# Performance work log

Measured on AMD Instinct MI355X. Metric: run time of the kernel, lower is better.

Reference implementation:

```python
import jax, jax.numpy as jnp
import numpy as np


def gcn_conv(x, edge_index, W, b):
    """PyG GCNConv: add self-loops, symmetric deg^{-1/2} normalization,
    linear transform, then scatter-add aggregation, plus bias."""
    n = x.shape[0]
    loops = jnp.arange(n, dtype=edge_index.dtype)
    src = jnp.concatenate([edge_index[0], loops])  # [E+N]
    dst = jnp.concatenate([edge_index[1], loops])
    ones = jnp.ones(src.shape[0], dtype=x.dtype)
    deg = jax.ops.segment_sum(ones, dst, num_segments=n)  # in-degree incl. self-loop
    dinv = jax.lax.rsqrt(jnp.maximum(deg, 1e-12))
    norm = dinv[src] * dinv[dst]  # [E+N]
    h = x @ W  # transform first (out_dim <= in_dim), [N, out]
    msg = h[src] * norm[:, None]  # gather + scale
    out = jax.ops.segment_sum(msg, dst, num_segments=n)  # scatter-add
    return out + b


def setup_inputs() -> dict:
    key = jax.random.key(0)
    ks = jax.random.split(key, 8)
    N, E, D_IN, D_OUT = 100000, 6400000, 32, 4
    x = jax.random.normal(ks[0], (N, D_IN), dtype=jnp.float32)
    edge_index = jax.random.randint(ks[1], (2, E), 0, N, dtype=jnp.int64)
    s1 = 1.0 / np.sqrt(D_IN)
    s2 = 1.0 / np.sqrt(16)
    s3 = 1.0 / np.sqrt(8)
    W1 = jax.random.uniform(ks[2], (D_IN, 16), jnp.float32, -s1, s1)
    b1 = jnp.zeros((16,), jnp.float32)
    W2 = jax.random.uniform(ks[3], (16, 8), jnp.float32, -s2, s2)
    b2 = jnp.zeros((8,), jnp.float32)
    Wfc = jax.random.uniform(ks[4], (8, D_OUT), jnp.float32, -s3, s3)
    bfc = jax.random.uniform(ks[5], (D_OUT,), jnp.float32, -s3, s3)
    return {"x": x, "edge_index": edge_index, "W1": W1, "b1": b1,
            "W2": W2, "b2": b2, "Wfc": Wfc, "bfc": bfc}


def reference(x, edge_index, W1, b1, W2, b2, Wfc, bfc):
    h = jax.nn.relu(gcn_conv(x, edge_index, W1, b1))
    h = jax.nn.relu(gcn_conv(h, edge_index, W2, b2))
    return h @ Wfc + bfc
```

## Files before the change

### kernel.cpp

```cpp
#include <hip/hip_runtime.h>
#include <hip/hip_fp16.h>

#define BLK 256
#define SHIFT 8
#define BSZ 256
#define MAXB 512
#define SRCBITS 17
#define SRCMASK ((1u << SRCBITS) - 1u)
#define TILE2 8192
#define BT 512
#define LCAP 18432


__global__ __launch_bounds__(BT) void k_binA2(const int* __restrict__ src,
                                              const int* __restrict__ dst, int E, int N,
                                              unsigned* __restrict__ binned,
                                              int* __restrict__ bofs) {
    __shared__ int cnt[MAXB];
    __shared__ int sscan[MAXB];
    __shared__ int excl[MAXB];
    __shared__ unsigned sw[TILE2];
    int t = threadIdx.x;
    cnt[t] = 0;
    __syncthreads();
    size_t tb = (size_t)blockIdx.x * TILE2;
    unsigned wv[16];
    int rkbk[16];
#pragma unroll
    for (int q = 0; q < 4; ++q) {
        int i4 = t + q * BT;
        size_t e0 = tb + (size_t)i4 * 4;
        int4 s4, d4;
        bool vec = (e0 + 4 <= (size_t)E);
        if (vec) {
            s4 = ((const int4*)src)[tb / 4 + i4];
            d4 = ((const int4*)dst)[tb / 4 + i4];
        }
#pragma unroll
        for (int j = 0; j < 4; ++j) {
            int idx = q * 4 + j;
            rkbk[idx] = -1;
            size_t e = e0 + j;
            int d = -1, s = -1;
            if (vec) {
                d = (j == 0) ? d4.x : (j == 1) ? d4.y : (j == 2) ? d4.z : d4.w;
                s = (j == 0) ? s4.x : (j == 1) ? s4.y : (j == 2) ? s4.z : s4.w;
            } else if (e < (size_t)E) {
                d = dst[e]; s = src[e];
            }
            if ((unsigned)d < (unsigned)N && (unsigned)s < (unsigned)N) {
                int b = d >> SHIFT;
                wv[idx] = (unsigned)s | ((unsigned)(d & (BSZ - 1)) << SRCBITS);
                int r = atomicAdd(&cnt[b], 1);
                rkbk[idx] = (r << 9) | b;
            }
        }
    }
    __syncthreads();
    sscan[t] = cnt[t];
    __syncthreads();
    for (int off = 1; off < MAXB; off <<= 1) {
        int u = (t >= off) ? sscan[t - off] : 0;
        __syncthreads();
        sscan[t] += u;
        __syncthreads();
    }
    excl[t] = sscan[t] - cnt[t];
    __syncthreads();
    int total = sscan[MAXB - 1];
#pragma unroll
    for (int idx = 0; idx < 16; ++idx) {
        int rb = rkbk[idx];
        if (rb >= 0) sw[excl[rb & 511] + (rb >> 9)] = wv[idx];
    }
    __syncthreads();
    for (int p = t; p < total; p += BT) binned[tb + p] = sw[p];
    size_t bo = (size_t)blockIdx.x * (MAXB + 1);
    bofs[bo + t] = excl[t];
    if (t == 0) bofs[bo + MAXB] = total;
}

__global__ __launch_bounds__(MAXB) void k_bsum(const int* __restrict__ bofs, int ntiles,
                                               int* __restrict__ btot) {
    int t = threadIdx.x;
    int c = 0;
    for (int tl = blockIdx.x; tl < ntiles; tl += gridDim.x) {
        size_t bo = (size_t)tl * (MAXB + 1);
        c += bofs[bo + t + 1] - bofs[bo + t];
    }
    if (c) atomicAdd(&btot[t], c);
}

__global__ __launch_bounds__(MAXB) void k_bscan(const int* __restrict__ btot,
                                                int* __restrict__ base) {
    __shared__ int s[MAXB];
    int t = threadIdx.x;
    int v = btot[t];
    s[t] = v;
    __syncthreads();
    for (int off = 1; off < MAXB; off <<= 1) {
        int u = (t >= off) ? s[t - off] : 0;
        __syncthreads();
        s[t] += u;
        __syncthreads();
    }
    base[t] = s[t] - v;
    if (t == MAXB - 1) base[MAXB] = s[t];
}


__global__ __launch_bounds__(1024) void k_buildB4(const unsigned* __restrict__ binned,
                                                  const int* __restrict__ bofs,
                                                  const int* __restrict__ baseB,
                                                  int ntiles, int N,
                                                  float* __restrict__ dinv,
                                                  int* __restrict__ rp,
                                                  unsigned* __restrict__ csr) {
    __shared__ int h[BSZ];
    __shared__ int sc[BSZ];
    __shared__ int cnt[BSZ];
    extern __shared__ unsigned lcsr[];
    int b = blockIdx.x;
    int t = threadIdx.x;
    int gb = b << SHIFT;
    if (t < BSZ) h[t] = 0;
    __syncthreads();
    int lane = t & 63, wid = t >> 6;
    int sub = lane >> 4, sl = lane & 15;
    for (int S = wid * 4 + sub; S < ntiles; S += 64) {
        size_t bo = (size_t)S * (MAXB + 1);
        int st = bofs[bo + b], en = bofs[bo + b + 1];
        size_t base = (size_t)S * TILE2;
        for (int k = st + sl; k < en; k += 16)
            atomicAdd(&h[binned[base + k] >> SRCBITS], 1);
    }
    __syncthreads();
    if (t < BSZ) sc[t] = h[t];
    __syncthreads();
    for (int off = 1; off < BSZ; off <<= 1) {
        int u = 0;
        if (t < BSZ && t >= off) u = sc[t - off];
        __syncthreads();
        if (t < BSZ) sc[t] += u;
        __syncthreads();
    }
    int bb = baseB[b];
    int total = sc[BSZ - 1];
    if (t < BSZ) {
        int v = h[t];
        int excl = sc[t] - v;
        int gnode = gb + t;
        if (gnode < N) {
            rp[gnode] = bb + excl;
            dinv[gnode] = rsqrtf((float)v + 1.0f);
        }
        if (t == BSZ - 1) {
            int endn = gb + BSZ;
            if (endn > N) endn = N;
            rp[endn] = bb + total;
        }
        cnt[t] = excl;
    }
    __syncthreads();
    bool big = (total > LCAP);
    for (int S = wid * 4 + sub; S < ntiles; S += 64) {
        size_t bo = (size_t)S * (MAXB + 1);
        int st = bofs[bo + b], en = bofs[bo + b + 1];
        size_t base = (size_t)S * TILE2;
        for (int k = st + sl; k < en; k += 16) {
            unsigned v = binned[base + k];
            int node = v >> SRCBITS;
            int pos = atomicAdd(&cnt[node], 1);
            if (!big) lcsr[pos] = v & SRCMASK;
            else      csr[bb + pos] = v & SRCMASK;
        }
    }
    __syncthreads();
    if (!big) {
        for (int p = t; p < total; p += 1024) csr[bb + p] = lcsr[p];
    }
}


union Pk8 { __half h[8]; uint4 u; };
union H2U { unsigned u; __half2 h; };

__global__ __launch_bounds__(BLK) void k_transform1h(const float* __restrict__ x,
                                                     const float* __restrict__ W1,
                                                     const float* __restrict__ dinv,
                                                     __half* __restrict__ g1h, int N) {
    __shared__ float sW[32 * 16];
    for (int t = threadIdx.x; t < 512; t += BLK) sW[t] = W1[t];
    __syncthreads();
    int i = blockIdx.x * BLK + threadIdx.x;
    if (i >= N) return;
    float xr[32];
    const float4* xp = (const float4*)(x + (size_t)i * 32);
#pragma unroll
    for (int q = 0; q < 8; ++q) {
        float4 v = xp[q];
        xr[4*q] = v.x; xr[4*q+1] = v.y; xr[4*q+2] = v.z; xr[4*q+3] = v.w;
    }
    float di = dinv[i];
    Pk8 p0, p1;
#pragma unroll
    for (int j = 0; j < 16; ++j) {
        float a = 0.f;
#pragma unroll
        for (int k = 0; k < 32; ++k) a += xr[k] * sW[k * 16 + j];
        if (j < 8) p0.h[j] = __float2half_rn(a * di);
        else       p1.h[j - 8] = __float2half_rn(a * di);
    }
    uint4* gp = (uint4*)(g1h + (size_t)i * 16);
    gp[0] = p0.u;
    gp[1] = p1.u;
}


__global__ __launch_bounds__(BLK) void k_agg1(const int* __restrict__ rp,
                                              const unsigned* __restrict__ csr,
                                              const __half* __restrict__ g1h,
                                              const float* __restrict__ dinv,
                                              const float* __restrict__ b1,
                                              const float* __restrict__ W2,
                                              float* __restrict__ g2, int N) {
    __shared__ float sW[16 * 8];
    __shared__ float sb[16];
    if (threadIdx.x < 128) sW[threadIdx.x] = W2[threadIdx.x];
    if (threadIdx.x < 16) sb[threadIdx.x] = b1[threadIdx.x];
    __syncthreads();
    int wid = blockIdx.x * (BLK / 64) + (threadIdx.x >> 6);
    if (wid >= N) return;
    int lane = threadIdx.x & 63;
    int c4 = lane & 3;
    int slot = lane >> 2;
    int base_ = rp[wid], end = rp[wid + 1];
    float a0 = 0.f, a1 = 0.f, a2 = 0.f, a3 = 0.f;
    int k = base_ + slot;
    for (; k + 16 < end; k += 32) {
        unsigned s0 = csr[k], s1 = csr[k + 16];
        uint2 u0 = *(const uint2*)(g1h + (size_t)s0 * 16 + (c4 << 2));
        uint2 u1 = *(const uint2*)(g1h + (size_t)s1 * 16 + (c4 << 2));
        H2U x0, x1, y0, y1;
        x0.u = u0.x; y0.u = u0.y; x1.u = u1.x; y1.u = u1.y;
        float2 f0 = __half22float2(x0.h), f1 = __half22float2(y0.h);
        float2 f2 = __half22float2(x1.h), f3 = __half22float2(y1.h);
        a0 += f0.x + f2.x; a1 += f0.y + f2.y;
        a2 += f1.x + f3.x; a3 += f1.y + f3.y;
    }
    if (k < end) {
        unsigned s0 = csr[k];
        uint2 u0 = *(const uint2*)(g1h + (size_t)s0 * 16 + (c4 << 2));
        H2U x0, y0;
        x0.u = u0.x; y0.u = u0.y;
        float2 f0 = __half22float2(x0.h), f1 = __half22float2(y0.h);
        a0 += f0.x; a1 += f0.y; a2 += f1.x; a3 += f1.y;
    }
#pragma unroll
    for (int m = 4; m <= 32; m <<= 1) {
        a0 += __shfl_xor(a0, m);
        a1 += __shfl_xor(a1, m);
        a2 += __shfl_xor(a2, m);
        a3 += __shfl_xor(a3, m);
    }
    float di = dinv[wid];
    uint2 su = *(const uint2*)(g1h + (size_t)wid * 16 + (c4 << 2));
    H2U sx, sy;
    sx.u = su.x; sy.u = su.y;
    float2 sf0 = __half22float2(sx.h), sf1 = __half22float2(sy.h);
    float hh[4];
    hh[0] = fmaxf((a0 + sf0.x) * di + sb[4*c4+0], 0.f);
    hh[1] = fmaxf((a1 + sf0.y) * di + sb[4*c4+1], 0.f);
    hh[2] = fmaxf((a2 + sf1.x) * di + sb[4*c4+2], 0.f);
    hh[3] = fmaxf((a3 + sf1.y) * di + sb[4*c4+3], 0.f);
    int g4 = lane & ~3;
    int o = lane & 7;
    float a = 0.f;
#pragma unroll
    for (int kk = 0; kk < 16; ++kk) {
        float hv = __shfl(hh[kk & 3], g4 + (kk >> 2));
        a += hv * sW[kk * 8 + o];
    }
    if (lane < 8) g2[(size_t)wid * 8 + lane] = a * di;
}

__global__ __launch_bounds__(BLK) void k_agg2(const int* __restrict__ rp,
                                              const unsigned* __restrict__ csr,
                                              const float* __restrict__ g2,
                                              const float* __restrict__ dinv,
                                              const float* __restrict__ b2,
                                              const float* __restrict__ Wfc,
                                              const float* __restrict__ bfc,
                                              float* __restrict__ out, int N) {
    __shared__ float sW[8 * 4];
    __shared__ float sb2[8];
    __shared__ float sbf[4];
    if (threadIdx.x < 32) sW[threadIdx.x] = Wfc[threadIdx.x];
    if (threadIdx.x < 8) sb2[threadIdx.x] = b2[threadIdx.x];
    if (threadIdx.x < 4) sbf[threadIdx.x] = bfc[threadIdx.x];
    __syncthreads();
    int wid = blockIdx.x * (BLK / 64) + (threadIdx.x >> 6);
    if (wid >= N) return;
    int lane = threadIdx.x & 63;
    int c4 = lane & 3;
    int slot = lane >> 2;
    int base_ = rp[wid], end = rp[wid + 1];
    float a0 = 0.f, a1 = 0.f;
    int k = base_ + slot;
    for (; k + 16 < end; k += 32) {
        unsigned s0 = csr[k], s1 = csr[k + 16];
        float2 f0 = *(const float2*)(g2 + (size_t)s0 * 8 + (c4 << 1));
        float2 f1 = *(const float2*)(g2 + (size_t)s1 * 8 + (c4 << 1));
        a0 += f0.x + f1.x;
        a1 += f0.y + f1.y;
    }
    if (k < end) {
        unsigned s0 = csr[k];
        float2 f0 = *(const float2*)(g2 + (size_t)s0 * 8 + (c4 << 1));
        a0 += f0.x; a1 += f0.y;
    }
#pragma unroll
    for (int m = 4; m <= 32; m <<= 1) {
        a0 += __shfl_xor(a0, m);
        a1 += __shfl_xor(a1, m);
    }
    float di = dinv[wid];
    float2 sf = *(const float2*)(g2 + (size_t)wid * 8 + (c4 << 1));
    float hh[2];
    hh[0] = fmaxf((a0 + sf.x) * di + sb2[2*c4+0], 0.f);
    hh[1] = fmaxf((a1 + sf.y) * di + sb2[2*c4+1], 0.f);
    int g4 = lane & ~3;
    int o = lane & 3;
    float a = 0.f;
#pragma unroll
    for (int j = 0; j < 8; ++j) {
        float hv = __shfl(hh[j & 1], g4 + (j >> 1));
        a += hv * sW[j * 4 + o];
    }
    if (lane < 4) out[(size_t)wid * 4 + lane] = a + sbf[lane];
}


__global__ __launch_bounds__(BLK) void k_count(const int* __restrict__ dst, int E, int N,
                                               float* __restrict__ cnt) {
    int i = blockIdx.x * BLK + threadIdx.x;
    if (i < E) {
        int d = dst[i];
        if ((unsigned)d < (unsigned)N) atomicAdd(&cnt[d], 1.0f);
    }
}
__global__ __launch_bounds__(BLK) void k_dinv_f(float* __restrict__ cnt, int N) {
    int i = blockIdx.x * BLK + threadIdx.x;
    if (i < N) cnt[i] = rsqrtf(cnt[i] + 1.0f);
}
__global__ __launch_bounds__(BLK) void k_transform1(const float* __restrict__ x,
                                                    const float* __restrict__ W1,
                                                    const float* __restrict__ dinv,
                                                    float* __restrict__ g1, int N) {
    __shared__ float sW[32 * 16];
    for (int t = threadIdx.x; t < 512; t += BLK) sW[t] = W1[t];
    __syncthreads();
    int i = blockIdx.x * BLK + threadIdx.x;
    if (i >= N) return;
    float xr[32];
    const float4* xp = (const float4*)(x + (size_t)i * 32);
#pragma unroll
    for (int q = 0; q < 8; ++q) {
        float4 v = xp[q];
        xr[4*q] = v.x; xr[4*q+1] = v.y; xr[4*q+2] = v.z; xr[4*q+3] = v.w;
    }
    float di = dinv[i];
    float o[16];
#pragma unroll
    for (int j = 0; j < 16; ++j) {
        float a = 0.f;
#pragma unroll
        for (int k = 0; k < 32; ++k) a += xr[k] * sW[k * 16 + j];
        o[j] = a * di;
    }
    float4* gp = (float4*)(g1 + (size_t)i * 16);
#pragma unroll
    for (int q = 0; q < 4; ++q)
        gp[q] = make_float4(o[4*q], o[4*q+1], o[4*q+2], o[4*q+3]);
}
template <int F>
__global__ __launch_bounds__(BLK) void k_edge_agg(const int* __restrict__ src,
                                                  const int* __restrict__ dst,
                                                  int E, int N,
                                                  const float* __restrict__ g,
                                                  float* __restrict__ agg) {
    size_t t = (size_t)blockIdx.x * BLK + threadIdx.x;
    int e = (int)(t / F);
    int f = (int)(t & (F - 1));
    if (e >= E) return;
    int s = src[e], d = dst[e];
    if ((unsigned)s >= (unsigned)N || (unsigned)d >= (unsigned)N) return;
    atomicAdd(&agg[(size_t)d * F + f], g[(size_t)s * F + f]);
}
__global__ __launch_bounds__(BLK) void k_node1(const float* __restrict__ g1,
                                               const float* __restrict__ agg1,
                                               const float* __restrict__ dinv,
                                               const float* __restrict__ b1,
                                               const float* __restrict__ W2,
                                               float* __restrict__ g2, int N) {
    __shared__ float sW[16 * 8];
    __shared__ float sb[16];
    for (int t = threadIdx.x; t < 128; t += BLK) sW[t] = W2[t];
    if (threadIdx.x < 16) sb[threadIdx.x] = b1[threadIdx.x];
    __syncthreads();
    int i = blockIdx.x * BLK + threadIdx.x;
    if (i >= N) return;
    float di = dinv[i];
    const float4* gp = (const float4*)(g1 + (size_t)i * 16);
    const float4* ap = (const float4*)(agg1 + (size_t)i * 16);
    float h[16];
#pragma unroll
    for (int q = 0; q < 4; ++q) {
        float4 gv = gp[q], av = ap[q];
        h[4*q+0] = fmaxf((av.x + gv.x) * di + sb[4*q+0], 0.f);
        h[4*q+1] = fmaxf((av.y + gv.y) * di + sb[4*q+1], 0.f);
        h[4*q+2] = fmaxf((av.z + gv.z) * di + sb[4*q+2], 0.f);
        h[4*q+3] = fmaxf((av.w + gv.w) * di + sb[4*q+3], 0.f);
    }
    float o[8];
#pragma unroll
    for (int j = 0; j < 8; ++j) {
        float a = 0.f;
#pragma unroll
        for (int k = 0; k < 16; ++k) a += h[k] * sW[k * 8 + j];
        o[j] = a * di;
    }
    float4* op = (float4*)(g2 + (size_t)i * 8);
    op[0] = make_float4(o[0], o[1], o[2], o[3]);
    op[1] = make_float4(o[4], o[5], o[6], o[7]);
}
__global__ __launch_bounds__(BLK) void k_node2(const float* __restrict__ g2,
                                               const float* __restrict__ agg2,
                                               const float* __restrict__ dinv,
                                               const float* __restrict__ b2,
                                               const float* __restrict__ Wfc,
                                               const float* __restrict__ bfc,
                                               float* __restrict__ out, int N) {
    __shared__ float sW[8 * 4];
    __shared__ float sb2[8];
    __shared__ float sbf[4];
    if (threadIdx.x < 32) sW[threadIdx.x] = Wfc[threadIdx.x];
    if (threadIdx.x < 8) sb2[threadIdx.x] = b2[threadIdx.x];
    if (threadIdx.x < 4) sbf[threadIdx.x] = bfc[threadIdx.x];
    __syncthreads();
    int i = blockIdx.x * BLK + threadIdx.x;
    if (i >= N) return;
    float di = dinv[i];
    const float4* gp = (const float4*)(g2 + (size_t)i * 8);
    const float4* ap = (const float4*)(agg2 + (size_t)i * 8);
    float h[8];
#pragma unroll
    for (int q = 0; q < 2; ++q) {
        float4 gv = gp[q], av = ap[q];
        h[4*q+0] = fmaxf((av.x + gv.x) * di + sb2[4*q+0], 0.f);
        h[4*q+1] = fmaxf((av.y + gv.y) * di + sb2[4*q+1], 0.f);
        h[4*q+2] = fmaxf((av.z + gv.z) * di + sb2[4*q+2], 0.f);
        h[4*q+3] = fmaxf((av.w + gv.w) * di + sb2[4*q+3], 0.f);
    }
    float o[4];
#pragma unroll
    for (int k = 0; k < 4; ++k) {
        float a = sbf[k];
#pragma unroll
        for (int j = 0; j < 8; ++j) a += h[j] * sW[j * 4 + k];
        o[k] = a;
    }
    ((float4*)(out + (size_t)i * 4))[0] = make_float4(o[0], o[1], o[2], o[3]);
}


extern "C" void kernel_launch(void* const* d_in, const int* in_sizes, int n_in,
                              void* d_out, int out_size, void* d_ws, size_t ws_size,
                              hipStream_t stream) {
    const float* x   = (const float*)d_in[0];
    const int*   ei  = (const int*)d_in[1];
    const float* W1  = (const float*)d_in[2];
    const float* b1  = (const float*)d_in[3];
    const float* W2  = (const float*)d_in[4];
    const float* b2  = (const float*)d_in[5];
    const float* Wfc = (const float*)d_in[6];
    const float* bfc = (const float*)d_in[7];

    int N = in_sizes[0] / 32;
    int E = in_sizes[1] / 2;
    const int* src = ei;
    const int* dst = ei + (size_t)E;

    int ntiles = (E + TILE2 - 1) / TILE2;
    int nbuk = (N + BSZ - 1) >> SHIFT;

    size_t w_g1h  = 0;
    size_t w_g2   = w_g1h + (size_t)8 * N;
    size_t w_dinv = w_g2 + (size_t)8 * N;
    size_t w_rp   = w_dinv + (size_t)N;
    size_t w_btot = w_rp + (size_t)N + 1;
    size_t w_bs   = w_btot + MAXB;
    size_t w_bofs = w_bs + MAXB + 1;
    size_t w_bin  = (w_bofs + (size_t)ntiles * (MAXB + 1) + 3) & ~(size_t)3;
    size_t w_csr  = w_bin + (size_t)E;
    size_t need   = (w_csr + (size_t)E) * 4;

    bool fast = (ws_size >= need) && (N <= (1 << SRCBITS)) && (nbuk <= MAXB);

    if (fast) {
        float*    ws     = (float*)d_ws;
        __half*   g1h    = (__half*)(ws + w_g1h);
        float*    g2     = ws + w_g2;
        float*    dinv   = ws + w_dinv;
        int*      rp     = (int*)(ws + w_rp);
        int*      btot   = (int*)(ws + w_btot);
        int*      baseB  = (int*)(ws + w_bs);
        int*      bofs   = (int*)(ws + w_bofs);
        unsigned* binned = (unsigned*)(ws + w_bin);
        unsigned* csr    = (unsigned*)(ws + w_csr);

        int nnode = (N + BLK - 1) / BLK;
        int nagg = (N + (BLK / 64) - 1) / (BLK / 64);

        hipMemsetAsync(btot, 0, MAXB * 4, stream);

        k_binA2<<<ntiles, BT, 0, stream>>>(src, dst, E, N, binned, bofs);
        k_bsum<<<128, MAXB, 0, stream>>>(bofs, ntiles, btot);
        k_bscan<<<1, MAXB, 0, stream>>>(btot, baseB);
        k_buildB4<<<nbuk, 1024, LCAP * 4, stream>>>(binned, bofs, baseB,
                                                    ntiles, N, dinv, rp, csr);
        k_transform1h<<<nnode, BLK, 0, stream>>>(x, W1, dinv, g1h, N);
        k_agg1<<<nagg, BLK, 0, stream>>>(rp, csr, g1h, dinv, b1, W2, g2, N);
        k_agg2<<<nagg, BLK, 0, stream>>>(rp, csr, g2, dinv, b2, Wfc, bfc,
                                         (float*)d_out, N);
    } else {
        float* ws   = (float*)d_ws;
        float* dinv = ws;
        float* g1   = dinv + (size_t)N;
        float* agg1 = g1 + (size_t)16 * N;
        float* g2   = agg1 + (size_t)16 * N;
        float* agg2 = g2 + (size_t)8 * N;

        hipMemsetAsync(dinv, 0, (size_t)N * 4, stream);
        hipMemsetAsync(agg1, 0, (size_t)16 * N * 4, stream);
        hipMemsetAsync(agg2, 0, (size_t)8 * N * 4, stream);

        k_count<<<(E + BLK - 1) / BLK, BLK, 0, stream>>>(dst, E, N, dinv);
        k_dinv_f<<<(N + BLK - 1) / BLK, BLK, 0, stream>>>(dinv, N);
        k_transform1<<<(N + BLK - 1) / BLK, BLK, 0, stream>>>(x, W1, dinv, g1, N);
        {
            size_t tot = (size_t)E * 16;
            k_edge_agg<16><<<(unsigned)((tot + BLK - 1) / BLK), BLK, 0, stream>>>(src, dst, E, N, g1, agg1);
        }
        k_node1<<<(N + BLK - 1) / BLK, BLK, 0, stream>>>(g1, agg1, dinv, b1, W2, g2, N);
        {
            size_t tot = (size_t)E * 8;
            k_edge_agg<8><<<(unsigned)((tot + BLK - 1) / BLK), BLK, 0, stream>>>(src, dst, E, N, g2, agg2);
        }
        k_node2<<<(N + BLK - 1) / BLK, BLK, 0, stream>>>(g2, agg2, dinv, b2, Wfc, bfc, (float*)d_out, N);
    }
}
```

Measured before the change: 190.3 us.

## Enlarge binning tiles, unroll CSR build, store byte offsets in CSR

Doubles the binning tile and block size, with guards so only the first 512 threads run the scan. Unrolls the histogram and scatter loops in the CSR build by two. Stores source indices pre-shifted as byte offsets (×32), so both aggregation kernels index the features with a plain byte add instead of a 64-bit multiply. The larger tile doubles LDS use per block and may lower occupancy. k_binA2 still holds only 16 edges per thread, so with 1024 threads it covers 16384 edges and matches the new tile.

```diff
diff --git a/kernel.cpp b/kernel.cpp
--- a/kernel.cpp
+++ b/kernel.cpp
@@ -7,8 +7,8 @@
 #define MAXB 512
 #define SRCBITS 17
 #define SRCMASK ((1u << SRCBITS) - 1u)
-#define TILE2 8192
-#define BT 512
+#define TILE2 16384
+#define BT 1024
 #define LCAP 18432
 
 
@@ -21,7 +21,7 @@
     __shared__ int excl[MAXB];
     __shared__ unsigned sw[TILE2];
     int t = threadIdx.x;
-    cnt[t] = 0;
+    if (t < MAXB) cnt[t] = 0;
     __syncthreads();
     size_t tb = (size_t)blockIdx.x * TILE2;
     unsigned wv[16];
@@ -57,15 +57,16 @@
         }
     }
     __syncthreads();
-    sscan[t] = cnt[t];
+    if (t < MAXB) sscan[t] = cnt[t];
     __syncthreads();
     for (int off = 1; off < MAXB; off <<= 1) {
-        int u = (t >= off) ? sscan[t - off] : 0;
+        int u = 0;
+        if (t < MAXB && t >= off) u = sscan[t - off];
         __syncthreads();
-        sscan[t] += u;
+        if (t < MAXB) sscan[t] += u;
         __syncthreads();
     }
-    excl[t] = sscan[t] - cnt[t];
+    if (t < MAXB) excl[t] = sscan[t] - cnt[t];
     __syncthreads();
     int total = sscan[MAXB - 1];
 #pragma unroll
@@ -76,7 +77,7 @@
     __syncthreads();
     for (int p = t; p < total; p += BT) binned[tb + p] = sw[p];
     size_t bo = (size_t)blockIdx.x * (MAXB + 1);
-    bofs[bo + t] = excl[t];
+    if (t < MAXB) bofs[bo + t] = excl[t];
     if (t == 0) bofs[bo + MAXB] = total;
 }
 
@@ -131,8 +132,14 @@
         size_t bo = (size_t)S * (MAXB + 1);
         int st = bofs[bo + b], en = bofs[bo + b + 1];
         size_t base = (size_t)S * TILE2;
-        for (int k = st + sl; k < en; k += 16)
-            atomicAdd(&h[binned[base + k] >> SRCBITS], 1);
+        int k = st + sl;
+        for (; k + 16 < en; k += 32) {
+            unsigned v0 = binned[base + k];
+            unsigned v1 = binned[base + k + 16];
+            atomicAdd(&h[v0 >> SRCBITS], 1);
+            atomicAdd(&h[v1 >> SRCBITS], 1);
+        }
+        if (k < en) atomicAdd(&h[binned[base + k] >> SRCBITS], 1);
     }
     __syncthreads();
     if (t < BSZ) sc[t] = h[t];
@@ -167,12 +174,23 @@
         size_t bo = (size_t)S * (MAXB + 1);
         int st = bofs[bo + b], en = bofs[bo + b + 1];
         size_t base = (size_t)S * TILE2;
-        for (int k = st + sl; k < en; k += 16) {
+        int k = st + sl;
+        for (; k + 16 < en; k += 32) {
+            unsigned v0 = binned[base + k];
+            unsigned v1 = binned[base + k + 16];
+            int p0 = atomicAdd(&cnt[v0 >> SRCBITS], 1);
+            int p1 = atomicAdd(&cnt[v1 >> SRCBITS], 1);
+            unsigned w0 = (v0 & SRCMASK) << 5;
+            unsigned w1 = (v1 & SRCMASK) << 5;
+            if (!big) { lcsr[p0] = w0; lcsr[p1] = w1; }
+            else      { csr[bb + p0] = w0; csr[bb + p1] = w1; }
+        }
+        if (k < en) {
             unsigned v = binned[base + k];
-            int node = v >> SRCBITS;
-            int pos = atomicAdd(&cnt[node], 1);
-            if (!big) lcsr[pos] = v & SRCMASK;
-            else      csr[bb + pos] = v & SRCMASK;
+            int pos = atomicAdd(&cnt[v >> SRCBITS], 1);
+            unsigned w = (v & SRCMASK) << 5;
+            if (!big) lcsr[pos] = w;
+            else      csr[bb + pos] = w;
         }
     }
     __syncthreads();
@@ -234,13 +252,15 @@
     int lane = threadIdx.x & 63;
     int c4 = lane & 3;
     int slot = lane >> 2;
+    const char* gbase = (const char*)g1h;
+    int foff = c4 << 3;
     int base_ = rp[wid], end = rp[wid + 1];
     float a0 = 0.f, a1 = 0.f, a2 = 0.f, a3 = 0.f;
     int k = base_ + slot;
     for (; k + 16 < end; k += 32) {
-        unsigned s0 = csr[k], s1 = csr[k + 16];
-        uint2 u0 = *(const uint2*)(g1h + (size_t)s0 * 16 + (c4 << 2));
-        uint2 u1 = *(const uint2*)(g1h + (size_t)s1 * 16 + (c4 << 2));
+        unsigned v0 = csr[k], v1 = csr[k + 16];
+        uint2 u0 = *(const uint2*)(gbase + v0 + foff);
+        uint2 u1 = *(const uint2*)(gbase + v1 + foff);
         H2U x0, x1, y0, y1;
         x0.u = u0.x; y0.u = u0.y; x1.u = u1.x; y1.u = u1.y;
         float2 f0 = __half22float2(x0.h), f1 = __half22float2(y0.h);
@@ -249,8 +269,8 @@
         a2 += f1.x + f3.x; a3 += f1.y + f3.y;
     }
     if (k < end) {
-        unsigned s0 = csr[k];
-        uint2 u0 = *(const uint2*)(g1h + (size_t)s0 * 16 + (c4 << 2));
+        unsigned v0 = csr[k];
+        uint2 u0 = *(const uint2*)(gbase + v0 + foff);
         H2U x0, y0;
         x0.u = u0.x; y0.u = u0.y;
         float2 f0 = __half22float2(x0.h), f1 = __half22float2(y0.h);
@@ -264,7 +284,7 @@
         a3 += __shfl_xor(a3, m);
     }
     float di = dinv[wid];
-    uint2 su = *(const uint2*)(g1h + (size_t)wid * 16 + (c4 << 2));
+    uint2 su = *(const uint2*)(gbase + ((size_t)wid << 5) + foff);
     H2U sx, sy;
     sx.u = su.x; sy.u = su.y;
     float2 sf0 = __half22float2(sx.h), sf1 = __half22float2(sy.h);
@@ -304,19 +324,21 @@
     int lane = threadIdx.x & 63;
     int c4 = lane & 3;
     int slot = lane >> 2;
+    const char* gbase = (const char*)g2;
+    int foff = c4 << 3;
     int base_ = rp[wid], end = rp[wid + 1];
     float a0 = 0.f, a1 = 0.f;
     int k = base_ + slot;
     for (; k + 16 < end; k += 32) {
-        unsigned s0 = csr[k], s1 = csr[k + 16];
-        float2 f0 = *(const float2*)(g2 + (size_t)s0 * 8 + (c4 << 1));
-        float2 f1 = *(const float2*)(g2 + (size_t)s1 * 8 + (c4 << 1));
+        unsigned v0 = csr[k], v1 = csr[k + 16];
+        float2 f0 = *(const float2*)(gbase + v0 + foff);
+        float2 f1 = *(const float2*)(gbase + v1 + foff);
         a0 += f0.x + f1.x;
         a1 += f0.y + f1.y;
     }
     if (k < end) {
-        unsigned s0 = csr[k];
-        float2 f0 = *(const float2*)(g2 + (size_t)s0 * 8 + (c4 << 1));
+        unsigned v0 = csr[k];
+        float2 f0 = *(const float2*)(gbase + v0 + foff);
         a0 += f0.x; a1 += f0.y;
     }
 #pragma unroll
@@ -325,7 +347,7 @@
         a1 += __shfl_xor(a1, m);
     }
     float di = dinv[wid];
-    float2 sf = *(const float2*)(g2 + (size_t)wid * 8 + (c4 << 1));
+    float2 sf = *(const float2*)(gbase + ((size_t)wid << 5) + foff);
     float hh[2];
     hh[0] = fmaxf((a0 + sf.x) * di + sb2[2*c4+0], 0.f);
     hh[1] = fmaxf((a1 + sf.y) * di + sb2[2*c4+1], 0.f);
```

Measured after the change: 180.5 us. -5.2%, faster.
